# Kernel tuning notes

Hardware: AMD Instinct MI355X
Metric: run time of the kernel (lower is better)

The kernel has to match this reference:

```python
import jax, jax.numpy as jnp
import numpy as np


def setup_inputs() -> dict:
    key = jax.random.key(0)
    k1, k2, k3 = jax.random.split(key, 3)
    N, C, H, W = 2048, 512, 7, 7
    HW = H * W
    x = jax.random.normal(k1, (N, C, H, W), dtype=jnp.float32)
    attn = jax.random.uniform(k2, (N, HW, HW), dtype=jnp.float32)
    D = jax.random.normal(k3, (N, HW, C), dtype=jnp.float32)
    alpha = jnp.ones((1,), dtype=jnp.float32)
    return {"x": x, "attn": attn, "D": D, "alpha": alpha}


def reference(x, attn, D, alpha):
    # out[n,c,p] = alpha * sum_q attn[n,p,q] * D[n,q,c] + x[n,c,p]
    N, C, H, W = x.shape
    HW = H * W
    # attn @ D -> [N, HW, C], then move channel to front: [N, C, HW]
    y = jnp.einsum('npq,nqc->ncp', attn, D)  # fused bmm + transpose
    out = x + alpha[0] * y.reshape(N, C, H, W)
    return out
```

## Files before the change

kernel.cpp:

```cpp
#include <hip/hip_runtime.h>

#define N_BATCH 2048
#define HW 49
#define CCH 512
#define PADP 52

__global__ __launch_bounds__(256) void transpose_attn(
    const float* __restrict__ attn, float* __restrict__ attnT)
{
    __shared__ float lds[HW * HW];
    const int n = blockIdx.x;
    const int tid = threadIdx.x;

    const float* a = attn + (size_t)n * (HW * HW);
    for (int i = tid; i < HW * HW; i += 256) lds[i] = a[i];
    __syncthreads();

    float* t = attnT + (size_t)n * (HW * PADP);
    for (int j = tid; j < HW * PADP; j += 256) {
        const int q = j / PADP;
        const int p = j - q * PADP;
        t[j] = (p < HW) ? lds[p * HW + q] : 0.0f;
    }
}

__global__ __launch_bounds__(256, 3) void fused_bmm_tn_add(
    const float* __restrict__ x, const float* __restrict__ D,
    const float* __restrict__ attnT, const float* __restrict__ alpha_p,
    float* __restrict__ out)
{
    __shared__ float ylds[256 * HW];
    const int n = blockIdx.x;
    const int tid = threadIdx.x;
    const int c0 = tid * 2;

    float acc0[PADP], acc1[PADP];
    #pragma unroll
    for (int p = 0; p < PADP; ++p) { acc0[p] = 0.f; acc1[p] = 0.f; }

    const float* Dn = D + (size_t)n * (HW * CCH);
    const float4* An = (const float4*)(attnT + (size_t)n * (HW * PADP));

    float2 d2 = *(const float2*)(Dn + c0);
    #pragma unroll 1
    for (int q = 0; q < HW; ++q) {
        float2 dnx = (q < HW - 1)
            ? *(const float2*)(Dn + (size_t)(q + 1) * CCH + c0)
            : make_float2(0.f, 0.f);
        const float4* Aq = An + q * (PADP / 4);
        #pragma unroll
        for (int j = 0; j < PADP / 4; ++j) {
            const float4 av = Aq[j];
            acc0[4*j+0] += av.x * d2.x;  acc1[4*j+0] += av.x * d2.y;
            acc0[4*j+1] += av.y * d2.x;  acc1[4*j+1] += av.y * d2.y;
            acc0[4*j+2] += av.z * d2.x;  acc1[4*j+2] += av.z * d2.y;
            acc0[4*j+3] += av.w * d2.x;  acc1[4*j+3] += av.w * d2.y;
        }
        d2 = dnx;
    }

    const float alpha = alpha_p[0];
    const size_t nbase = (size_t)n * (CCH * HW);

    #pragma unroll 1
    for (int ch = 0; ch < 2; ++ch) {
        __syncthreads();
        if (tid >= ch * 128 && tid < ch * 128 + 128) {
            const int cl = c0 - ch * 256;
            #pragma unroll
            for (int p = 0; p < HW; ++p) {
                ylds[cl * HW + p]       = acc0[p];
                ylds[(cl + 1) * HW + p] = acc1[p];
            }
        }
        __syncthreads();
        const float4* x4 = (const float4*)(x + nbase + (size_t)ch * (256 * HW));
        float4*       o4 = (float4*)(out + nbase + (size_t)ch * (256 * HW));
        const float4* y4 = (const float4*)ylds;
        for (int i = tid; i < (256 * HW) / 4; i += 256) {
            const float4 xv = x4[i];
            const float4 yv = y4[i];
            float4 ov;
            ov.x = xv.x + alpha * yv.x;
            ov.y = xv.y + alpha * yv.y;
            ov.z = xv.z + alpha * yv.z;
            ov.w = xv.w + alpha * yv.w;
            o4[i] = ov;
        }
    }
}

extern "C" void kernel_launch(void* const* d_in, const int* in_sizes, int n_in,
                              void* d_out, int out_size, void* d_ws, size_t ws_size,
                              hipStream_t stream) {
    const float* x     = (const float*)d_in[0];
    const float* attn  = (const float*)d_in[1];
    const float* Dm    = (const float*)d_in[2];
    const float* alpha = (const float*)d_in[3];
    float* out = (float*)d_out;

    float* attnT = (float*)d_ws;

    transpose_attn<<<N_BATCH, 256, 0, stream>>>(attn, attnT);
    fused_bmm_tn_add<<<N_BATCH, 256, 0, stream>>>(x, Dm, attnT, alpha, out);
}
```

Before: 619.2 us.

## Restructure bmm as per-channel row dot products with split channel halves

The main kernel now gives each thread one channel. It keeps that channel's 49 D values in registers and, for each output row p, takes a dot product with the padded attention row, prefetching the next row. The grid doubles to two blocks per batch, each covering 256 channels, so there is more parallelism and the staged two-pass LDS epilogue goes away. The pre-kernel only pads attn rows instead of transposing them, and output stores are nontemporal. The cost is a horizontal reduction per row and D loads that are strided across q, although they stay coalesced across threads.

```diff
diff --git a/kernel.cpp b/kernel.cpp
--- a/kernel.cpp
+++ b/kernel.cpp
@@ -3,90 +3,81 @@
 #define N_BATCH 2048
 #define HW 49
 #define CCH 512
-#define PADP 52
+#define PADQ 52
 
-__global__ __launch_bounds__(256) void transpose_attn(
-    const float* __restrict__ attn, float* __restrict__ attnT)
+typedef float f4 __attribute__((ext_vector_type(4)));
+
+__global__ __launch_bounds__(256) void pad_attn(
+    const float* __restrict__ attn, float* __restrict__ attnP)
 {
-    __shared__ float lds[HW * HW];
     const int n = blockIdx.x;
     const int tid = threadIdx.x;
-
     const float* a = attn + (size_t)n * (HW * HW);
-    for (int i = tid; i < HW * HW; i += 256) lds[i] = a[i];
-    __syncthreads();
-
-    float* t = attnT + (size_t)n * (HW * PADP);
-    for (int j = tid; j < HW * PADP; j += 256) {
-        const int q = j / PADP;
-        const int p = j - q * PADP;
-        t[j] = (p < HW) ? lds[p * HW + q] : 0.0f;
+    float* t = attnP + (size_t)n * (HW * PADQ);
+    for (int j = tid; j < HW * PADQ; j += 256) {
+        const int p = j / PADQ;
+        const int q = j - p * PADQ;
+        t[j] = (q < HW) ? a[p * HW + q] : 0.0f;
     }
 }
 
-__global__ __launch_bounds__(256, 3) void fused_bmm_tn_add(
+__global__ __launch_bounds__(256, 3) void fused_bmm_rowdot_add(
     const float* __restrict__ x, const float* __restrict__ D,
-    const float* __restrict__ attnT, const float* __restrict__ alpha_p,
+    const float* __restrict__ attnP, const float* __restrict__ alpha_p,
     float* __restrict__ out)
 {
     __shared__ float ylds[256 * HW];
-    const int n = blockIdx.x;
+    const int bid = blockIdx.x;
+    const int n   = bid >> 1;
+    const int h   = bid & 1;
     const int tid = threadIdx.x;
-    const int c0 = tid * 2;
+    const int c   = h * 256 + tid;
 
-    float acc0[PADP], acc1[PADP];
+    float d[PADQ];
+    d[PADQ - 3] = 0.0f; d[PADQ - 2] = 0.0f; d[PADQ - 1] = 0.0f;
+    const float* Dn = D + (size_t)n * (HW * CCH) + c;
     #pragma unroll
-    for (int p = 0; p < PADP; ++p) { acc0[p] = 0.f; acc1[p] = 0.f; }
+    for (int q = 0; q < HW; ++q) d[q] = Dn[(size_t)q * CCH];
 
-    const float* Dn = D + (size_t)n * (HW * CCH);
-    const float4* An = (const float4*)(attnT + (size_t)n * (HW * PADP));
+    const f4* Af = (const f4*)(attnP + (size_t)n * (HW * PADQ));
 
-    float2 d2 = *(const float2*)(Dn + c0);
+    f4 aC[PADQ / 4];
+    #pragma unroll
+    for (int j = 0; j < PADQ / 4; ++j) aC[j] = Af[j];
+
     #pragma unroll 1
-    for (int q = 0; q < HW; ++q) {
-        float2 dnx = (q < HW - 1)
-            ? *(const float2*)(Dn + (size_t)(q + 1) * CCH + c0)
-            : make_float2(0.f, 0.f);
-        const float4* Aq = An + q * (PADP / 4);
+    for (int p = 0; p < HW; ++p) {
+        const int pn = (p + 1 < HW) ? (p + 1) : p;
+        f4 aN[PADQ / 4];
         #pragma unroll
-        for (int j = 0; j < PADP / 4; ++j) {
-            const float4 av = Aq[j];
-            acc0[4*j+0] += av.x * d2.x;  acc1[4*j+0] += av.x * d2.y;
-            acc0[4*j+1] += av.y * d2.x;  acc1[4*j+1] += av.y * d2.y;
-            acc0[4*j+2] += av.z * d2.x;  acc1[4*j+2] += av.z * d2.y;
-            acc0[4*j+3] += av.w * d2.x;  acc1[4*j+3] += av.w * d2.y;
+        for (int j = 0; j < PADQ / 4; ++j) aN[j] = Af[pn * (PADQ / 4) + j];
+
+        float s0 = 0.f, s1 = 0.f, s2 = 0.f, s3 = 0.f;
+        #pragma unroll
+        for (int j = 0; j < PADQ / 4; ++j) {
+            s0 += aC[j].x * d[4 * j + 0];
+            s1 += aC[j].y * d[4 * j + 1];
+            s2 += aC[j].z * d[4 * j + 2];
+            s3 += aC[j].w * d[4 * j + 3];
         }
-        d2 = dnx;
+        ylds[tid * HW + p] = (s0 + s1) + (s2 + s3);
+
+        #pragma unroll
+        for (int j = 0; j < PADQ / 4; ++j) aC[j] = aN[j];
     }
 
+    __syncthreads();
+
     const float alpha = alpha_p[0];
-    const size_t nbase = (size_t)n * (CCH * HW);
-
-    #pragma unroll 1
-    for (int ch = 0; ch < 2; ++ch) {
-        __syncthreads();
-        if (tid >= ch * 128 && tid < ch * 128 + 128) {
-            const int cl = c0 - ch * 256;
-            #pragma unroll
-            for (int p = 0; p < HW; ++p) {
-                ylds[cl * HW + p]       = acc0[p];
-                ylds[(cl + 1) * HW + p] = acc1[p];
-            }
-        }
-        __syncthreads();
-        const float4* x4 = (const float4*)(x + nbase + (size_t)ch * (256 * HW));
-        float4*       o4 = (float4*)(out + nbase + (size_t)ch * (256 * HW));
-        const float4* y4 = (const float4*)ylds;
-        for (int i = tid; i < (256 * HW) / 4; i += 256) {
-            const float4 xv = x4[i];
-            const float4 yv = y4[i];
-            float4 ov;
-            ov.x = xv.x + alpha * yv.x;
-            ov.y = xv.y + alpha * yv.y;
-            ov.z = xv.z + alpha * yv.z;
-            ov.w = xv.w + alpha * yv.w;
-            o4[i] = ov;
-        }
+    const size_t base = (size_t)n * (CCH * HW) + (size_t)h * (256 * HW);
+    const f4* x4 = (const f4*)(x + base);
+    f4*       o4 = (f4*)(out + base);
+    const f4* y4 = (const f4*)ylds;
+    for (int i = tid; i < (256 * HW) / 4; i += 256) {
+        const f4 xv = x4[i];
+        const f4 yv = y4[i];
+        f4 ov = xv + alpha * yv;
+        __builtin_nontemporal_store(ov, &o4[i]);
     }
 }
 
@@ -99,8 +90,8 @@
     const float* alpha = (const float*)d_in[3];
     float* out = (float*)d_out;
 
-    float* attnT = (float*)d_ws;
+    float* attnP = (float*)d_ws;
 
-    transpose_attn<<<N_BATCH, 256, 0, stream>>>(attn, attnT);
-    fused_bmm_tn_add<<<N_BATCH, 256, 0, stream>>>(x, Dm, attnT, alpha, out);
+    pad_attn<<<N_BATCH, 256, 0, stream>>>(attn, attnP);
+    fused_bmm_rowdot_add<<<N_BATCH * 2, 256, 0, stream>>>(x, Dm, attnP, alpha, out);
 }
```

Result: slower. 650.2 us (+5.0%).
